# Kernel tuning notes

Measured on AMD Instinct MI355X. Metric: run time of the kernel, lower is better.

Reference implementation:

```python
import jax, jax.numpy as jnp
import numpy as np
import math

IN_F, OUT_F, GRID = 1024, 1024, 7
BATCH, SEQ = 4, 4096


def _l2norm(v, eps=1e-12):
    return v / (jnp.linalg.norm(v) + eps)


def setup_inputs() -> dict:
    key = jax.random.key(0)
    k0, k1, k2, k3 = jax.random.split(key, 4)
    x = jax.random.normal(k0, (BATCH, SEQ, IN_F), dtype=jnp.float32)
    # spectral-normed base linear (weights nonzero for a meaningful baseline)
    base_w = jax.random.normal(k1, (OUT_F, IN_F), dtype=jnp.float32) * 0.02
    base_b = jnp.zeros((OUT_F,), dtype=jnp.float32)
    u = jax.random.normal(k2, (OUT_F,), dtype=jnp.float32)  # power-iteration buffer
    # Chebyshev translation points and fixed logspace scales (as in __init__)
    steps = jnp.arange(GRID, dtype=jnp.float32)
    translation = (-jnp.cos((2.0 * steps + 1.0) / (2.0 * GRID) * math.pi) * 1.5).reshape(1, 1, GRID)
    scale = (1.0 * jnp.logspace(-0.5, 0.5, GRID)).reshape(1, 1, GRID).astype(jnp.float32)
    wavelet_w = jax.random.normal(k3, (OUT_F, IN_F * GRID), dtype=jnp.float32) * 0.01
    soft_threshold = jnp.array([0.005], dtype=jnp.float32)
    output_scale = jnp.array([1.0], dtype=jnp.float32)
    return dict(x=x, base_w=base_w, base_b=base_b, u=u, translation=translation,
                scale=scale, wavelet_w=wavelet_w, soft_threshold=soft_threshold,
                output_scale=output_scale)


def reference(x, base_w, base_b, u, translation, scale, wavelet_w, soft_threshold, output_scale):
    x_flat = x.reshape(-1, x.shape[-1])  # [N, IN]
    # spectral norm: one power iteration (no grad through u, v), sigma = u' W v
    v = jax.lax.stop_gradient(_l2norm(base_w.T @ u))
    u2 = jax.lax.stop_gradient(_l2norm(base_w @ v))
    sigma = u2 @ (base_w @ v)
    w_sn = base_w / sigma
    base_out = jax.nn.silu(x_flat) @ w_sn.T + base_b  # [N, OUT]
    # wavelet (Ricker) basis expansion
    safe_scale = jnp.maximum(jnp.abs(scale), 0.1)  # [1,1,G]
    x_norm = jnp.tanh(x_flat) * 2.5  # [N, IN]
    xe = (x_norm[:, :, None] - translation) / safe_scale  # [N, IN, G]
    basis = (1.0 - xe * xe) * jnp.exp(-0.5 * xe * xe)
    kan = basis.reshape(x_flat.shape[0], -1) @ wavelet_w.T  # [N, OUT]
    thr = jax.nn.softplus(soft_threshold)
    kan = jnp.sign(kan) * jax.nn.relu(jnp.abs(kan) - thr)
    out = (base_out + kan) * output_scale
    return out.reshape(*x.shape[:-1], wavelet_w.shape[0])
```

## Files before the change

kernel.cpp:

```cpp
#include <hip/hip_runtime.h>
#include <math.h>


typedef __attribute__((ext_vector_type(4))) float  f32x4;
typedef __attribute__((ext_vector_type(8))) __bf16 bf16x8;
typedef __attribute__((ext_vector_type(8))) unsigned short u16x8;

#define NROWS 16384
#define INF   1024
#define OUTF  1024
#define GG    7
#define KKAN  7168
#define KTOT  8192

static __device__ __forceinline__ unsigned short f2bf(float f) {
  union { float f; unsigned int u; } v; v.f = f;
  unsigned int r = v.u + 0x7fffu + ((v.u >> 16) & 1u);
  return (unsigned short)(r >> 16);
}

__global__ void zero_t(float* __restrict__ t) { t[threadIdx.x] = 0.f; }

__global__ void wtu_acc(const float* __restrict__ W, const float* __restrict__ u,
                        float* __restrict__ t) {
  int tid = threadIdx.x;
  int j4 = tid * 4;
  int i0 = blockIdx.x * 16;
  f32x4 acc = {0.f, 0.f, 0.f, 0.f};
  for (int i = i0; i < i0 + 16; ++i) {
    float ui = u[i];
    f32x4 w4 = *(const f32x4*)(W + (size_t)i * INF + j4);
    acc[0] += w4[0] * ui; acc[1] += w4[1] * ui;
    acc[2] += w4[2] * ui; acc[3] += w4[3] * ui;
  }
  atomicAdd(&t[j4 + 0], acc[0]);
  atomicAdd(&t[j4 + 1], acc[1]);
  atomicAdd(&t[j4 + 2], acc[2]);
  atomicAdd(&t[j4 + 3], acc[3]);
}

__global__ void mv_w_t(const float* __restrict__ W, const float* __restrict__ t,
                       float* __restrict__ s) {
  int i = blockIdx.x;
  int tid = threadIdx.x;
  float p = 0.f;
  for (int j = tid; j < INF; j += 256) p += W[(size_t)i * INF + j] * t[j];
  __shared__ float red[256];
  red[tid] = p; __syncthreads();
  for (int k = 128; k > 0; k >>= 1) { if (tid < k) red[tid] += red[tid + k]; __syncthreads(); }
  if (tid == 0) s[i] = red[0];
}

__global__ void sigma_finish(const float* __restrict__ t, const float* __restrict__ s,
                             const float* __restrict__ st, const float* __restrict__ os,
                             float* __restrict__ scal) {
  __shared__ float r1[256], r2[256];
  int tid = threadIdx.x;
  float p1 = 0.f, p2 = 0.f;
  for (int i = tid; i < 1024; i += 256) { float a = t[i]; p1 += a * a; float b = s[i]; p2 += b * b; }
  r1[tid] = p1; r2[tid] = p2; __syncthreads();
  for (int k = 128; k > 0; k >>= 1) { if (tid < k) { r1[tid] += r1[tid + k]; r2[tid] += r2[tid + k]; } __syncthreads(); }
  if (tid == 0) {
    float nt = sqrtf(r1[0]);
    float ns = sqrtf(r2[0]);
    float nq = ns / (nt + 1e-12f);
    float sigma = nq * nq / (nq + 1e-12f);
    scal[0] = 1.f / sigma;
    scal[1] = log1pf(__expf(st[0]));
    scal[2] = os[0];
  }
}

__global__ void wsn_cast(const float* __restrict__ w, const float* __restrict__ scal,
                         unsigned short* __restrict__ Wp) {
  float is = scal[0];
  int idx = blockIdx.x * 256 + threadIdx.x;
  int row = idx >> 7, i0 = (idx & 127) << 3;
  const f32x4* p = (const f32x4*)(w + (size_t)row * INF + i0);
  f32x4 a = p[0], b = p[1];
  u16x8 v;
  v[0] = f2bf(a[0] * is); v[1] = f2bf(a[1] * is); v[2] = f2bf(a[2] * is); v[3] = f2bf(a[3] * is);
  v[4] = f2bf(b[0] * is); v[5] = f2bf(b[1] * is); v[6] = f2bf(b[2] * is); v[7] = f2bf(b[3] * is);
  *(u16x8*)(Wp + (size_t)row * KTOT + KKAN + i0) = v;
}

__global__ void wkan_cast(const float* __restrict__ w, unsigned short* __restrict__ Wp) {
  __shared__ float row[KKAN];
  int orow = blockIdx.x;
  const float* src = w + (size_t)orow * KKAN;
  for (int c = threadIdx.x * 4; c < KKAN; c += 1024)
    *(f32x4*)&row[c] = *(const f32x4*)&src[c];
  __syncthreads();
  unsigned short* dst = Wp + (size_t)orow * KTOT;
  for (int r = threadIdx.x; r < 896; r += 256) {
    int g = r >> 7, i0 = (r & 127) << 3;
    u16x8 v;
#pragma unroll
    for (int j = 0; j < 8; j++) v[j] = f2bf(row[(i0 + j) * GG + g]);
    *(u16x8*)(dst + g * 1024 + i0) = v;
  }
}

__global__ void expand_kernel(const float* __restrict__ x,
                              const float* __restrict__ translation,
                              const float* __restrict__ scale,
                              unsigned short* __restrict__ Ap,
                              int row0, int nrows) {
  float tr[GG], iss[GG];
#pragma unroll
  for (int g = 0; g < GG; g++) {
    tr[g] = translation[g];
    float s = fabsf(scale[g]);
    iss[g] = 1.f / (s < 0.1f ? 0.1f : s);
  }
  int units = nrows * (INF / 8);
  int stride = gridDim.x * blockDim.x;
  for (int uu = blockIdx.x * blockDim.x + threadIdx.x; uu < units; uu += stride) {
    int nloc = uu >> 7;
    int i0 = (uu & 127) << 3;
    const f32x4* xp = (const f32x4*)(x + (size_t)(row0 + nloc) * INF + i0);
    f32x4 xa = xp[0], xb = xp[1];
    float xv[8] = {xa[0], xa[1], xa[2], xa[3], xb[0], xb[1], xb[2], xb[3]};
    u16x8 sb, kb[GG];
#pragma unroll
    for (int j = 0; j < 8; j++) {
      float xx = xv[j];
      float si = xx / (1.f + __expf(-xx));
      sb[j] = f2bf(si);
      float e2 = __expf(2.f * xx);
      float xn = 2.5f * (1.f - 2.f / (e2 + 1.f));
#pragma unroll
      for (int g = 0; g < GG; g++) {
        float xe = (xn - tr[g]) * iss[g];
        float t2 = xe * xe;
        float b = (1.f - t2) * __expf(-0.5f * t2);
        kb[g][j] = f2bf(b);
      }
    }
    unsigned short* rp = Ap + (size_t)nloc * KTOT;
    *(u16x8*)(rp + KKAN + i0) = sb;
#pragma unroll
    for (int g = 0; g < GG; g++) *(u16x8*)(rp + g * 1024 + i0) = kb[g];
  }
}

static __device__ __forceinline__ void gload16(const unsigned short* g, unsigned short* l) {
  __builtin_amdgcn_global_load_lds(
      (const __attribute__((address_space(1))) unsigned int*)g,
      (__attribute__((address_space(3))) unsigned int*)l, 16, 0, 0);
}

#define SCB   __builtin_amdgcn_sched_barrier(0)
#define SBAR  do { SCB; __builtin_amdgcn_s_barrier(); } while (0)
#define VM(N) asm volatile("s_waitcnt vmcnt(" #N ")" ::: "memory")
#define LG(N) asm volatile("s_waitcnt lgkmcnt(" #N ")" ::: "memory")

#define STAGE(db, tt) do { \
    const unsigned short* _sa = gA + (size_t)(tt) * 64; \
    const unsigned short* _sb = gB + (size_t)(tt) * 64; \
    unsigned short* _da = ldsS + (db) * 24576; \
    unsigned short* _db2 = ldsS + (db) * 24576 + 16384; \
    _Pragma("unroll") for (int r = 0; r < 8; ++r) \
      gload16(_sa + (size_t)(r * 32) * KTOT, _da + r * 2048); \
    _Pragma("unroll") for (int r = 0; r < 4; ++r) \
      gload16(_sb + (size_t)(r * 32) * KTOT, _db2 + r * 2048); \
  } while (0)

#define RD12(FA, FB, bb, kx) do { \
    _Pragma("unroll") for (int i = 0; i < 8; ++i) \
      FA[i] = *(const bf16x8*)(pA + (bb) * 49152 + i * 2048 + (kx)); \
    _Pragma("unroll") for (int j = 0; j < 4; ++j) \
      FB[j] = *(const bf16x8*)(pB + (bb) * 49152 + j * 2048 + (kx)); \
  } while (0)

#define MM32h(FA, FB) do { _Pragma("unroll") for (int i = 0; i < 8; ++i) \
    _Pragma("unroll") for (int j = 0; j < 4; ++j) \
      acc[i][j] = __builtin_amdgcn_mfma_f32_16x16x32_bf16(FA[i], FB[j], acc[i][j], 0, 0, 0); } while (0)

#define TILE(tt, bb, nb, db, SS, NR, W1) do { \
    RD12(fYA, fYB, bb, kx1); \
    SCB; \
    if (SS) STAGE(db, (tt) + 2); \
    SCB; \
    __builtin_amdgcn_s_setprio(1); MM32h(fXA, fXB); __builtin_amdgcn_s_setprio(0); \
    LG(0); SCB; \
    W1; \
    SBAR; \
    if (NR) { RD12(fXA, fXB, nb, kx0); SCB; } \
    __builtin_amdgcn_s_setprio(1); MM32h(fYA, fYB); __builtin_amdgcn_s_setprio(0); \
    LG(0); SCB; \
  } while (0)

__global__ __launch_bounds__(256, 1) void gemm_k(
    const unsigned short* __restrict__ A,
    const unsigned short* __restrict__ W,
    const float* __restrict__ bias,
    const float* __restrict__ scal,
    float* __restrict__ out) {
  __shared__ unsigned short lds[73728];

  int bid = blockIdx.x;
  int cpx = gridDim.x >> 3;
  int swz = (bid & 7) * cpx + (bid >> 3);
  int m0 = (swz >> 3) * 256;
  int n0 = (swz & 7) * 128;
  int tid = threadIdx.x;
  int wv = tid >> 6, l = tid & 63;
  int wr = wv >> 1, wc = wv & 1;

  float thr = scal[1], osc = scal[2];

  int rowq = tid >> 3;
  int swk = ((tid & 7) ^ (rowq & 7)) << 3;
  const unsigned short* gA = A + (size_t)(m0 + rowq) * KTOT + swk;
  const unsigned short* gB = W + (size_t)(n0 + rowq) * KTOT + swk;
  unsigned short* ldsS = lds + wv * 512;

  int lr = l & 15;
  int kb = (l >> 4) << 4;
  int xr = (l & 7) << 4;
  int kx0 = kb ^ xr;
  int kx1 = (64 | kb) ^ xr;
  const char* pA = (const char*)lds + (wr * 128 + lr) * 128;
  const char* pB = (const char*)lds + 32768 + (wc * 64 + lr) * 128;

  bf16x8 fXA[8], fXB[4], fYA[8], fYB[4];
  f32x4 acc[8][4] = {};

  STAGE(0, 0);
  STAGE(1, 1);
  VM(12);
  SBAR;
  RD12(fXA, fXB, 0, kx0);
  LG(0); SCB;

  for (int t = 0; t < 108; t += 3) {
    TILE(t,     0, 1, 2, 1, 1, VM(12));
    TILE(t + 1, 1, 2, 0, 1, 1, VM(12));
    TILE(t + 2, 2, 0, 1, 1, 1, VM(12));
  }
  TILE(108, 0, 1, 2, 1, 1, VM(12));
  TILE(109, 1, 2, 0, 1, 1, VM(12));
  TILE(110, 2, 0, 1, 1, 1, VM(12));
  TILE(111, 0, 1, 2, 1, 1, VM(12));

#pragma unroll
  for (int i = 0; i < 8; ++i)
#pragma unroll
    for (int j = 0; j < 4; ++j)
#pragma unroll
      for (int e = 0; e < 4; ++e) {
        float v = acc[i][j][e];
        float a = fabsf(v) - thr;
        a = a > 0.f ? a : 0.f;
        acc[i][j][e] = v > 0.f ? a : -a;
      }

  TILE(112, 1, 2, 0, 1, 1, VM(12));
  TILE(113, 2, 0, 1, 1, 1, VM(12));
  TILE(114, 0, 1, 2, 1, 1, VM(12));
  TILE(115, 1, 2, 0, 1, 1, VM(12));
  TILE(116, 2, 0, 1, 1, 1, VM(12));
  TILE(117, 0, 1, 2, 1, 1, VM(12));
  TILE(118, 1, 2, 0, 1, 1, VM(12));
  TILE(119, 2, 0, 1, 1, 1, VM(12));
  TILE(120, 0, 1, 2, 1, 1, VM(12));
  TILE(121, 1, 2, 0, 1, 1, VM(12));
  TILE(122, 2, 0, 1, 1, 1, VM(12));
  TILE(123, 0, 1, 2, 1, 1, VM(12));
  TILE(124, 1, 2, 0, 1, 1, VM(12));
  TILE(125, 2, 0, 1, 1, 1, VM(12));
  TILE(126, 0, 1, 2, 0, 1, VM(0));
  TILE(127, 1, 2, 0, 0, 0, (void)0);

  int rr = m0 + wr * 128 + ((l >> 4) << 2);
  int cc = n0 + wc * 64 + lr;
#pragma unroll
  for (int i = 0; i < 8; ++i)
#pragma unroll
    for (int j = 0; j < 4; ++j) {
      int c = cc + j * 16;
      float bc = bias[c];
#pragma unroll
      for (int e = 0; e < 4; ++e) {
        int r = rr + i * 16 + e;
        out[(size_t)r * OUTF + c] = (acc[i][j][e] + bc) * osc;
      }
    }
}

extern "C" void kernel_launch(void* const* d_in, const int* in_sizes, int n_in,
                              void* d_out, int out_size, void* d_ws, size_t ws_size,
                              hipStream_t stream) {
  const float* x              = (const float*)d_in[0];
  const float* base_w         = (const float*)d_in[1];
  const float* base_b         = (const float*)d_in[2];
  const float* u              = (const float*)d_in[3];
  const float* translation    = (const float*)d_in[4];
  const float* scale          = (const float*)d_in[5];
  const float* wavelet_w      = (const float*)d_in[6];
  const float* soft_threshold = (const float*)d_in[7];
  const float* output_scale   = (const float*)d_in[8];
  float* out = (float*)d_out;

  char* ws = (char*)d_ws;
  float* t_vec = (float*)ws;
  float* s_vec = t_vec + 1024;
  float* scal  = s_vec + 1024;
  unsigned short* Wp = (unsigned short*)(ws + 16384);
  char* dynbuf = ws + 16384 + (size_t)KTOT * OUTF * 2;

  size_t fixed = 16384 + (size_t)KTOT * OUTF * 2;
  size_t avail = ws_size > fixed ? ws_size - fixed : 0;

  zero_t<<<1, 1024, 0, stream>>>(t_vec);
  wtu_acc<<<64, 256, 0, stream>>>(base_w, u, t_vec);
  mv_w_t<<<1024, 256, 0, stream>>>(base_w, t_vec, s_vec);
  sigma_finish<<<1, 256, 0, stream>>>(t_vec, s_vec, soft_threshold, output_scale, scal);
  wsn_cast<<<512, 256, 0, stream>>>(base_w, scal, Wp);
  wkan_cast<<<1024, 256, 0, stream>>>(wavelet_w, Wp);

  const size_t ROW = (size_t)KTOT * 2;
  size_t total = (size_t)NROWS * ROW;
  int nch = (int)((total + (avail > 0 ? avail : 1) - 1) / (avail > 0 ? avail : 1));
  if (nch < 1) nch = 1;
  long mc = (((NROWS + nch - 1) / nch) + 255) & ~255L;
  while (mc > 256 && (size_t)mc * ROW > avail) mc -= 256;
  if (mc < 256) mc = 256;

  unsigned short* Ap = (unsigned short*)dynbuf;

  for (long r0 = 0; r0 < NROWS; r0 += mc) {
    long nr = (NROWS - r0 < mc) ? (NROWS - r0) : mc;
    expand_kernel<<<2048, 256, 0, stream>>>(x, translation, scale, Ap, (int)r0, (int)nr);
    int mt = (int)(nr / 256);
    gemm_k<<<mt * 8, 256, 0, stream>>>(Ap, Wp, base_b, scal, out + (size_t)r0 * OUTF);
  }
}
```

Baseline: 373.7 us.

## Fuse Ricker basis expansion into GEMM via producer/consumer warp specialization

Drops the separate expand kernel and its materialised bf16 A matrix (16384x8192). The GEMM now runs 512 threads per block. Four producer waves load x, compute tanh, the Ricker basis and silu per K-tile, and write bf16 tiles into swizzled LDS. Four consumer waves stream weight tiles and run the MFMAs. The weight layout is reordered so each 64-wide K tile holds one grid index for 64 input features, which lets the producers recompute from a small x slice. The cost is that x and its transcendentals are recomputed for every output-column tile (8 times), and there is a barrier-lockstepped double buffer with only two stages.

```diff
diff --git a/kernel.cpp b/kernel.cpp
--- a/kernel.cpp
+++ b/kernel.cpp
@@ -5,6 +5,7 @@
 typedef __attribute__((ext_vector_type(4))) float  f32x4;
 typedef __attribute__((ext_vector_type(8))) __bf16 bf16x8;
 typedef __attribute__((ext_vector_type(8))) unsigned short u16x8;
+typedef __attribute__((ext_vector_type(4))) unsigned int u32x4;
 
 #define NROWS 16384
 #define INF   1024
@@ -97,50 +98,7 @@
     u16x8 v;
 #pragma unroll
     for (int j = 0; j < 8; j++) v[j] = f2bf(row[(i0 + j) * GG + g]);
-    *(u16x8*)(dst + g * 1024 + i0) = v;
-  }
-}
-
-__global__ void expand_kernel(const float* __restrict__ x,
-                              const float* __restrict__ translation,
-                              const float* __restrict__ scale,
-                              unsigned short* __restrict__ Ap,
-                              int row0, int nrows) {
-  float tr[GG], iss[GG];
-#pragma unroll
-  for (int g = 0; g < GG; g++) {
-    tr[g] = translation[g];
-    float s = fabsf(scale[g]);
-    iss[g] = 1.f / (s < 0.1f ? 0.1f : s);
-  }
-  int units = nrows * (INF / 8);
-  int stride = gridDim.x * blockDim.x;
-  for (int uu = blockIdx.x * blockDim.x + threadIdx.x; uu < units; uu += stride) {
-    int nloc = uu >> 7;
-    int i0 = (uu & 127) << 3;
-    const f32x4* xp = (const f32x4*)(x + (size_t)(row0 + nloc) * INF + i0);
-    f32x4 xa = xp[0], xb = xp[1];
-    float xv[8] = {xa[0], xa[1], xa[2], xa[3], xb[0], xb[1], xb[2], xb[3]};
-    u16x8 sb, kb[GG];
-#pragma unroll
-    for (int j = 0; j < 8; j++) {
-      float xx = xv[j];
-      float si = xx / (1.f + __expf(-xx));
-      sb[j] = f2bf(si);
-      float e2 = __expf(2.f * xx);
-      float xn = 2.5f * (1.f - 2.f / (e2 + 1.f));
-#pragma unroll
-      for (int g = 0; g < GG; g++) {
-        float xe = (xn - tr[g]) * iss[g];
-        float t2 = xe * xe;
-        float b = (1.f - t2) * __expf(-0.5f * t2);
-        kb[g][j] = f2bf(b);
-      }
-    }
-    unsigned short* rp = Ap + (size_t)nloc * KTOT;
-    *(u16x8*)(rp + KKAN + i0) = sb;
-#pragma unroll
-    for (int g = 0; g < GG; g++) *(u16x8*)(rp + g * 1024 + i0) = kb[g];
+    *(u16x8*)(dst + ((i0 >> 6) * 7 + g) * 64 + (i0 & 63)) = v;
   }
 }
 
@@ -155,138 +113,180 @@
 #define VM(N) asm volatile("s_waitcnt vmcnt(" #N ")" ::: "memory")
 #define LG(N) asm volatile("s_waitcnt lgkmcnt(" #N ")" ::: "memory")
 
-#define STAGE(db, tt) do { \
-    const unsigned short* _sa = gA + (size_t)(tt) * 64; \
-    const unsigned short* _sb = gB + (size_t)(tt) * 64; \
-    unsigned short* _da = ldsS + (db) * 24576; \
-    unsigned short* _db2 = ldsS + (db) * 24576 + 16384; \
-    _Pragma("unroll") for (int r = 0; r < 8; ++r) \
-      gload16(_sa + (size_t)(r * 32) * KTOT, _da + r * 2048); \
-    _Pragma("unroll") for (int r = 0; r < 4; ++r) \
-      gload16(_sb + (size_t)(r * 32) * KTOT, _db2 + r * 2048); \
+#define BGLOAD(bb, tt) do { \
+    const unsigned short* _s = gB + (size_t)(tt) * 64; \
+    unsigned short* _d = lds + (bb) * 24576 + 16384 + wv * 512; \
+    _Pragma("unroll") for (int r_ = 0; r_ < 4; ++r_) \
+      gload16(_s + (size_t)(r_ * 32) * KTOT, _d + r_ * 2048); \
   } while (0)
 
-#define RD12(FA, FB, bb, kx) do { \
+#define RD12(kx, bb) do { \
     _Pragma("unroll") for (int i = 0; i < 8; ++i) \
       FA[i] = *(const bf16x8*)(pA + (bb) * 49152 + i * 2048 + (kx)); \
     _Pragma("unroll") for (int j = 0; j < 4; ++j) \
       FB[j] = *(const bf16x8*)(pB + (bb) * 49152 + j * 2048 + (kx)); \
   } while (0)
 
-#define MM32h(FA, FB) do { _Pragma("unroll") for (int i = 0; i < 8; ++i) \
+#define MM32 do { _Pragma("unroll") for (int i = 0; i < 8; ++i) \
     _Pragma("unroll") for (int j = 0; j < 4; ++j) \
       acc[i][j] = __builtin_amdgcn_mfma_f32_16x16x32_bf16(FA[i], FB[j], acc[i][j], 0, 0, 0); } while (0)
 
-#define TILE(tt, bb, nb, db, SS, NR, W1) do { \
-    RD12(fYA, fYB, bb, kx1); \
-    SCB; \
-    if (SS) STAGE(db, (tt) + 2); \
-    SCB; \
-    __builtin_amdgcn_s_setprio(1); MM32h(fXA, fXB); __builtin_amdgcn_s_setprio(0); \
-    LG(0); SCB; \
-    W1; \
-    SBAR; \
-    if (NR) { RD12(fXA, fXB, nb, kx0); SCB; } \
-    __builtin_amdgcn_s_setprio(1); MM32h(fYA, fYB); __builtin_amdgcn_s_setprio(0); \
-    LG(0); SCB; \
+#define XLOADP(ICOL, TANH) do { \
+    _Pragma("unroll") for (int w_ = 0; w_ < 8; ++w_) { \
+      const f32x4* _p = (const f32x4*)(xbase + (size_t)(prow + w_ * 32) * 1024 + (ICOL) + pc * 8); \
+      xd[w_][0] = _p[0]; xd[w_][1] = _p[1]; \
+    } \
+    if (TANH) { \
+      _Pragma("unroll") for (int w_ = 0; w_ < 8; ++w_) \
+      _Pragma("unroll") for (int h_ = 0; h_ < 2; ++h_) \
+      _Pragma("unroll") for (int e_ = 0; e_ < 4; ++e_) { \
+        float v_ = xd[w_][h_][e_]; \
+        float e2_ = __expf(2.f * v_); \
+        xd[w_][h_][e_] = 2.5f * (1.f - 2.f / (e2_ + 1.f)); \
+      } \
+    } \
   } while (0)
 
-__global__ __launch_bounds__(256, 1) void gemm_k(
-    const unsigned short* __restrict__ A,
+#define CWPROD(bb, IS_, NT_, SILU) do { \
+    unsigned short* _wb = lds + (bb) * 24576; \
+    _Pragma("unroll") for (int w_ = 0; w_ < 8; ++w_) { \
+      int row_ = prow + w_ * 32; \
+      float bv[8]; \
+      _Pragma("unroll") for (int e_ = 0; e_ < 8; ++e_) { \
+        float v_ = (e_ < 4) ? xd[w_][0][e_] : xd[w_][1][e_ - 4]; \
+        if (SILU) { bv[e_] = v_ / (1.f + __expf(-v_)); } \
+        else { float xe_ = fmaf(v_, IS_, NT_); float t2_ = xe_ * xe_; \
+               bv[e_] = (1.f - t2_) * __expf(-0.5f * t2_); } \
+      } \
+      unsigned int o0, o1, o2, o3; \
+      asm("v_cvt_pk_bf16_f32 %0, %1, %2" : "=v"(o0) : "v"(bv[0]), "v"(bv[1])); \
+      asm("v_cvt_pk_bf16_f32 %0, %1, %2" : "=v"(o1) : "v"(bv[2]), "v"(bv[3])); \
+      asm("v_cvt_pk_bf16_f32 %0, %1, %2" : "=v"(o2) : "v"(bv[4]), "v"(bv[5])); \
+      asm("v_cvt_pk_bf16_f32 %0, %1, %2" : "=v"(o3) : "v"(bv[6]), "v"(bv[7])); \
+      u32x4 w4_ = {o0, o1, o2, o3}; \
+      *(u32x4*)(_wb + row_ * 64 + ((pc ^ (row_ & 7)) << 3)) = w4_; \
+    } \
+  } while (0)
+
+__global__ __launch_bounds__(512, 2) void gemm_k(
+    const float* __restrict__ x,
     const unsigned short* __restrict__ W,
     const float* __restrict__ bias,
     const float* __restrict__ scal,
+    const float* __restrict__ trP,
+    const float* __restrict__ scP,
     float* __restrict__ out) {
-  __shared__ unsigned short lds[73728];
+  __shared__ unsigned short lds[49184];
+  float* ldsF = (float*)(lds + 49152);
 
   int bid = blockIdx.x;
-  int cpx = gridDim.x >> 3;
-  int swz = (bid & 7) * cpx + (bid >> 3);
-  int m0 = (swz >> 3) * 256;
-  int n0 = (swz & 7) * 128;
+  int swz = (bid & 7) * 64 + (bid >> 3);
+  int n0 = (swz >> 6) * 128;
+  int m0 = (swz & 63) * 256;
   int tid = threadIdx.x;
   int wv = tid >> 6, l = tid & 63;
-  int wr = wv >> 1, wc = wv & 1;
+  bool cons = wv < 4;
+  int wr = (wv >> 1) & 1, wc = wv & 1;
 
   float thr = scal[1], osc = scal[2];
 
-  int rowq = tid >> 3;
-  int swk = ((tid & 7) ^ (rowq & 7)) << 3;
-  const unsigned short* gA = A + (size_t)(m0 + rowq) * KTOT + swk;
-  const unsigned short* gB = W + (size_t)(n0 + rowq) * KTOT + swk;
-  unsigned short* ldsS = lds + wv * 512;
+  int rowqB = tid >> 3;
+  int swkB = ((tid & 7) ^ (rowqB & 7)) << 3;
+  const unsigned short* gB = W + (size_t)(n0 + (rowqB & 31)) * KTOT + swkB;
 
   int lr = l & 15;
-  int kb = (l >> 4) << 4;
-  int xr = (l & 7) << 4;
-  int kx0 = kb ^ xr;
-  int kx1 = (64 | kb) ^ xr;
+  int kx0 = (((l >> 4) << 4) ^ ((l & 7) << 4));
+  int kx1 = kx0 ^ 64;
   const char* pA = (const char*)lds + (wr * 128 + lr) * 128;
   const char* pB = (const char*)lds + 32768 + (wc * 64 + lr) * 128;
 
-  bf16x8 fXA[8], fXB[4], fYA[8], fYB[4];
+  int pt = tid & 255;
+  int prow = pt >> 3;
+  int pc = pt & 7;
+  const float* xbase = x + (size_t)m0 * 1024;
+
+  bf16x8 FA[8], FB[4];
+  f32x4 xd[8][2];
   f32x4 acc[8][4] = {};
 
-  STAGE(0, 0);
-  STAGE(1, 1);
-  VM(12);
+  if (tid < 7) {
+    float s = fabsf(scP[tid]);
+    s = s < 0.1f ? 0.1f : s;
+    ldsF[tid] = 1.f / s;
+    ldsF[7 + tid] = -trP[tid] / s;
+  }
+  __syncthreads();
+
+  if (cons) {
+    BGLOAD(0, 0);
+    VM(0);
+  } else {
+    XLOADP(0, 1);
+    CWPROD(0, ldsF[0], ldsF[7], 0);
+    LG(0);
+  }
   SBAR;
-  RD12(fXA, fXB, 0, kx0);
-  LG(0); SCB;
-
-  for (int t = 0; t < 108; t += 3) {
-    TILE(t,     0, 1, 2, 1, 1, VM(12));
-    TILE(t + 1, 1, 2, 0, 1, 1, VM(12));
-    TILE(t + 2, 2, 0, 1, 1, 1, VM(12));
-  }
-  TILE(108, 0, 1, 2, 1, 1, VM(12));
-  TILE(109, 1, 2, 0, 1, 1, VM(12));
-  TILE(110, 2, 0, 1, 1, 1, VM(12));
-  TILE(111, 0, 1, 2, 1, 1, VM(12));
-
-#pragma unroll
-  for (int i = 0; i < 8; ++i)
-#pragma unroll
-    for (int j = 0; j < 4; ++j)
-#pragma unroll
-      for (int e = 0; e < 4; ++e) {
-        float v = acc[i][j][e];
-        float a = fabsf(v) - thr;
-        a = a > 0.f ? a : 0.f;
-        acc[i][j][e] = v > 0.f ? a : -a;
+
+  int pg = 1, picol = 0;
+
+#pragma unroll 2
+  for (int t = 0; t < 128; ++t) {
+    int b = t & 1;
+    if (cons) {
+      RD12(kx0, b);
+      if (t < 127) BGLOAD(b ^ 1, t + 1);
+      LG(0); SCB;
+      __builtin_amdgcn_s_setprio(1); MM32; __builtin_amdgcn_s_setprio(0);
+      RD12(kx1, b);
+      LG(0); SCB;
+      __builtin_amdgcn_s_setprio(1); MM32; __builtin_amdgcn_s_setprio(0);
+      if (t < 127) VM(0);
+      SBAR;
+      if (t == 111) {
+#pragma unroll
+        for (int i = 0; i < 8; ++i)
+#pragma unroll
+          for (int j = 0; j < 4; ++j)
+#pragma unroll
+            for (int e = 0; e < 4; ++e) {
+              float v = acc[i][j][e];
+              float a = fabsf(v) - thr;
+              a = a > 0.f ? a : 0.f;
+              acc[i][j][e] = v > 0.f ? a : -a;
+            }
       }
-
-  TILE(112, 1, 2, 0, 1, 1, VM(12));
-  TILE(113, 2, 0, 1, 1, 1, VM(12));
-  TILE(114, 0, 1, 2, 1, 1, VM(12));
-  TILE(115, 1, 2, 0, 1, 1, VM(12));
-  TILE(116, 2, 0, 1, 1, 1, VM(12));
-  TILE(117, 0, 1, 2, 1, 1, VM(12));
-  TILE(118, 1, 2, 0, 1, 1, VM(12));
-  TILE(119, 2, 0, 1, 1, 1, VM(12));
-  TILE(120, 0, 1, 2, 1, 1, VM(12));
-  TILE(121, 1, 2, 0, 1, 1, VM(12));
-  TILE(122, 2, 0, 1, 1, 1, VM(12));
-  TILE(123, 0, 1, 2, 1, 1, VM(12));
-  TILE(124, 1, 2, 0, 1, 1, VM(12));
-  TILE(125, 2, 0, 1, 1, 1, VM(12));
-  TILE(126, 0, 1, 2, 0, 1, VM(0));
-  TILE(127, 1, 2, 0, 0, 0, (void)0);
-
-  int rr = m0 + wr * 128 + ((l >> 4) << 2);
-  int cc = n0 + wc * 64 + lr;
-#pragma unroll
-  for (int i = 0; i < 8; ++i)
-#pragma unroll
-    for (int j = 0; j < 4; ++j) {
-      int c = cc + j * 16;
-      float bc = bias[c];
-#pragma unroll
-      for (int e = 0; e < 4; ++e) {
-        int r = rr + i * 16 + e;
-        out[(size_t)r * OUTF + c] = (acc[i][j][e] + bc) * osc;
+    } else {
+      if (t < 111) {
+        if (pg == 0) XLOADP(picol, 1);
+        float is_ = ldsF[pg], nt_ = ldsF[7 + pg];
+        CWPROD(b ^ 1, is_, nt_, 0);
+        pg = (pg == 6) ? 0 : pg + 1;
+        if (pg == 0) picol += 64;
+      } else if (t < 127) {
+        XLOADP((t - 111) * 64, 0);
+        CWPROD(b ^ 1, 0.f, 0.f, 1);
       }
+      LG(0);
+      SBAR;
     }
+  }
+
+  if (cons) {
+    int rr = m0 + wr * 128 + ((l >> 4) << 2);
+    int cc = n0 + wc * 64 + lr;
+#pragma unroll
+    for (int i = 0; i < 8; ++i)
+#pragma unroll
+      for (int j = 0; j < 4; ++j) {
+        int c = cc + j * 16;
+        float bc = bias[c];
+#pragma unroll
+        for (int e = 0; e < 4; ++e) {
+          int r = rr + i * 16 + e;
+          out[(size_t)r * OUTF + c] = (acc[i][j][e] + bc) * osc;
+        }
+      }
+  }
 }
 
 extern "C" void kernel_launch(void* const* d_in, const int* in_sizes, int n_in,
@@ -308,10 +308,6 @@
   float* s_vec = t_vec + 1024;
   float* scal  = s_vec + 1024;
   unsigned short* Wp = (unsigned short*)(ws + 16384);
-  char* dynbuf = ws + 16384 + (size_t)KTOT * OUTF * 2;
-
-  size_t fixed = 16384 + (size_t)KTOT * OUTF * 2;
-  size_t avail = ws_size > fixed ? ws_size - fixed : 0;
 
   zero_t<<<1, 1024, 0, stream>>>(t_vec);
   wtu_acc<<<64, 256, 0, stream>>>(base_w, u, t_vec);
@@ -320,20 +316,5 @@
   wsn_cast<<<512, 256, 0, stream>>>(base_w, scal, Wp);
   wkan_cast<<<1024, 256, 0, stream>>>(wavelet_w, Wp);
 
-  const size_t ROW = (size_t)KTOT * 2;
-  size_t total = (size_t)NROWS * ROW;
-  int nch = (int)((total + (avail > 0 ? avail : 1) - 1) / (avail > 0 ? avail : 1));
-  if (nch < 1) nch = 1;
-  long mc = (((NROWS + nch - 1) / nch) + 255) & ~255L;
-  while (mc > 256 && (size_t)mc * ROW > avail) mc -= 256;
-  if (mc < 256) mc = 256;
-
-  unsigned short* Ap = (unsigned short*)dynbuf;
-
-  for (long r0 = 0; r0 < NROWS; r0 += mc) {
-    long nr = (NROWS - r0 < mc) ? (NROWS - r0) : mc;
-    expand_kernel<<<2048, 256, 0, stream>>>(x, translation, scale, Ap, (int)r0, (int)nr);
-    int mt = (int)(nr / 256);
-    gemm_k<<<mt * 8, 256, 0, stream>>>(Ap, Wp, base_b, scal, out + (size_t)r0 * OUTF);
-  }
-}
+  gemm_k<<<512, 512, 0, stream>>>(x, Wp, base_b, scal, translation, scale, out);
+}
```

After: 777.4 us. 2.08x slower.
